# Kernel tuning notes

Measured on AMD Instinct MI355X. Metric: run time of the kernel, lower is better.

## Reference

```python
import jax, jax.numpy as jnp
import numpy as np

DIM = 512
HEADS = 8
DIM_HEAD = 64
INNER = HEADS * DIM_HEAD


def setup_inputs() -> dict:
    key = jax.random.key(0)
    k1, k2, k3, k4 = jax.random.split(key, 4)
    x = jax.random.normal(k1, (4, 8192, DIM), dtype=jnp.float32)
    # nn.Linear(dim, inner*3, bias=False): weight applied as x @ W^T; store transposed form [dim, 3*inner]
    w_qkv = jax.random.normal(k2, (DIM, 3 * INNER), dtype=jnp.float32) / np.sqrt(DIM)
    w_out = jax.random.normal(k3, (INNER, DIM), dtype=jnp.float32) / np.sqrt(INNER)
    b_out = jax.random.normal(k4, (DIM,), dtype=jnp.float32) * 0.01
    return {"x": x, "w_qkv": w_qkv, "w_out": w_out, "b_out": b_out}


def reference(x, w_qkv, w_out, b_out):
    b, n, d = x.shape
    qkv = x @ w_qkv  # [b, n, 3*inner]
    q, k, v = jnp.split(qkv, 3, axis=-1)

    def to_heads(t):
        return t.reshape(b, n, HEADS, DIM_HEAD).transpose(0, 2, 1, 3)  # [b,h,n,dh]

    q, k, v = map(to_heads, (q, k, v))
    q = jax.nn.elu(q) + 1.0
    k = jax.nn.elu(k) + 1.0
    # kv summary: [b,h,dh,dh]
    kv = jnp.einsum('bhnd,bhnm->bhdm', k, v)
    # normalizer z: [b,h,n]  (note: original does NOT apply self.scale)
    z = 1.0 / (jnp.einsum('bhnd,bhd->bhn', q, k.sum(axis=2)) + 1e-6)
    out = jnp.einsum('bhnd,bhdm->bhnm', q, kv) * z[..., None]  # [b,h,n,dh]
    out = out.transpose(0, 2, 1, 3).reshape(b, n, INNER)
    return out @ w_out + b_out
```

## Files before the change

### kernel.cpp

```cpp
#include <hip/hip_runtime.h>
#include <hip/hip_bf16.h>

#define B_SZ 4
#define SEQ 8192
#define DIM 512
#define HEADS 8
#define DH 64
#define INNER 512
#define QKV_COLS 1536
#define M_TOT (B_SZ * SEQ)
#define BHN (B_SZ * HEADS)

typedef __bf16 bf16x8 __attribute__((ext_vector_type(8)));
typedef __bf16 bf16x4 __attribute__((ext_vector_type(4)));
typedef float f32x4 __attribute__((ext_vector_type(4)));

__device__ __forceinline__ float elu1(float x) {
    return x > 0.f ? x + 1.f : __expf(x);
}

__device__ __forceinline__ void gl_lds16(const void* g, void* l) {
    __builtin_amdgcn_global_load_lds(
        (const __attribute__((address_space(1))) unsigned int*)g,
        (__attribute__((address_space(3))) unsigned int*)l, 16, 0, 0);
}

__global__ void convert_x(const float* __restrict__ x, __bf16* __restrict__ xb) {
    int id = blockIdx.x * 256 + threadIdx.x;
    float4 f = reinterpret_cast<const float4*>(x)[id];
    bf16x4 h = {(__bf16)f.x, (__bf16)f.y, (__bf16)f.z, (__bf16)f.w};
    reinterpret_cast<bf16x4*>(xb)[id] = h;
}

__global__ void convert_weights(const float* __restrict__ w_qkv,
                                const float* __restrict__ w_out,
                                __bf16* __restrict__ wqkv_t,
                                __bf16* __restrict__ wout_t) {
    int id = blockIdx.x * 256 + threadIdx.x;
    if (id < QKV_COLS * DIM) {
        int n = id / DIM, k = id % DIM;
        wqkv_t[id] = (__bf16)w_qkv[k * QKV_COLS + n];
    } else {
        int id2 = id - QKV_COLS * DIM;
        if (id2 < INNER * DIM) {
            int n = id2 / DIM, k = id2 % DIM;
            wout_t[id2] = (__bf16)w_out[k * DIM + n];
        }
    }
}

#define TSTR 136
__launch_bounds__(256, 2)
__global__ void gemm_qkv(const __bf16* __restrict__ xb,
                         const __bf16* __restrict__ wqkv_t,
                         __bf16* __restrict__ q_ws,
                         __bf16* __restrict__ kT_ws,
                         __bf16* __restrict__ vT_ws) {
    __shared__ __attribute__((aligned(16))) char smem[128 * TSTR * 2];
    __bf16* As = (__bf16*)smem;
    __bf16* Bs = (__bf16*)(smem + 16384);
    __bf16* T  = (__bf16*)smem;

    const int tid = threadIdx.x;
    const int wid = tid >> 6;
    const int lane = tid & 63;
    const int wm = wid >> 1, wn = wid & 1;
    const int lq = lane >> 4, lr = lane & 15;
    const int m0 = blockIdx.x * 128;
    const int n0 = blockIdx.y * 128;
    const int lrow = lane >> 3;
    const int lcol = (lane & 7) * 8;

    f32x4 acc[4][4] = {};

    for (int kb = 0; kb < DIM; kb += 64) {
#pragma unroll
        for (int t = 0; t < 4; ++t) {
            int qi = wid * 4 + t;
            int row = qi * 8 + lrow;
            gl_lds16(&xb[(size_t)(m0 + row) * DIM + kb + lcol], &As[qi * 512]);
            gl_lds16(&wqkv_t[(size_t)(n0 + row) * DIM + kb + lcol], &Bs[qi * 512]);
        }
        __syncthreads();
#pragma unroll
        for (int ks = 0; ks < 2; ++ks) {
            bf16x8 af[4], bfv[4];
#pragma unroll
            for (int i = 0; i < 4; ++i)
                af[i] = *reinterpret_cast<const bf16x8*>(
                    &As[(wm * 64 + i * 16 + lr) * 64 + ks * 32 + lq * 8]);
#pragma unroll
            for (int j = 0; j < 4; ++j)
                bfv[j] = *reinterpret_cast<const bf16x8*>(
                    &Bs[(wn * 64 + j * 16 + lr) * 64 + ks * 32 + lq * 8]);
#pragma unroll
            for (int i = 0; i < 4; ++i)
#pragma unroll
                for (int j = 0; j < 4; ++j)
                    acc[i][j] = __builtin_amdgcn_mfma_f32_16x16x32_bf16(
                        af[i], bfv[j], acc[i][j], 0, 0, 0);
        }
        __syncthreads();
    }

    const int which = n0 / INNER;
    const int n0w = n0 % INNER;
    const int b = m0 / SEQ;
    const int nbase = m0 % SEQ;

    if (which == 0) {
#pragma unroll
        for (int i = 0; i < 4; ++i)
#pragma unroll
            for (int j = 0; j < 4; ++j) {
                int col = wn * 64 + j * 16 + lr;
#pragma unroll
                for (int r = 0; r < 4; ++r)
                    T[(wm * 64 + i * 16 + lq * 4 + r) * TSTR + col] =
                        (__bf16)elu1(acc[i][j][r]);
            }
        __syncthreads();
#pragma unroll
        for (int it = 0; it < 8; ++it) {
            int c = tid + it * 256;
            int row = c >> 4, dc = (c & 15) * 8;
            bf16x8 v = *reinterpret_cast<const bf16x8*>(&T[row * TSTR + dc]);
            int col = n0w + dc;
            int h = col >> 6, d = col & 63;
            *reinterpret_cast<bf16x8*>(
                &q_ws[(((size_t)(b * HEADS + h)) * SEQ + nbase + row) * DH + d]) = v;
        }
    } else {
        __bf16* dst = (which == 1) ? kT_ws : vT_ws;
#pragma unroll
        for (int i = 0; i < 4; ++i)
#pragma unroll
            for (int j = 0; j < 4; ++j) {
                int col = wn * 64 + j * 16 + lr;
                int rowb = wm * 64 + i * 16 + lq * 4;
                bf16x4 h4;
#pragma unroll
                for (int r = 0; r < 4; ++r) {
                    float v = acc[i][j][r];
                    h4[r] = (__bf16)((which == 1) ? elu1(v) : v);
                }
                *reinterpret_cast<bf16x4*>(&T[col * TSTR + rowb]) = h4;
            }
        __syncthreads();
#pragma unroll
        for (int it = 0; it < 8; ++it) {
            int c = tid + it * 256;
            int colIdx = c >> 4, rc = (c & 15) * 8;
            bf16x8 v = *reinterpret_cast<const bf16x8*>(&T[colIdx * TSTR + rc]);
            int gcol = n0w + colIdx;
            int h = gcol >> 6, d = gcol & 63;
            *reinterpret_cast<bf16x8*>(
                &dst[(((size_t)(b * HEADS + h)) * DH + d) * SEQ + nbase + rc]) = v;
        }
    }
}

__launch_bounds__(256, 2)
__global__ void kv_reduce(const __bf16* __restrict__ kT,
                          const __bf16* __restrict__ vT,
                          float* __restrict__ kv_t) {
    __shared__ __attribute__((aligned(16))) __bf16 Ks[64][136];
    __shared__ __attribute__((aligned(16))) __bf16 Vs[64][136];
    const int tid = threadIdx.x;
    const int wid = tid >> 6;
    const int lane = tid & 63;
    const int lq = lane >> 4, lr = lane & 15;
    const int bh = blockIdx.y;
    const int n0 = blockIdx.x * 512;
    const size_t base = (size_t)bh * DH * SEQ;
    f32x4 acc[4] = {};

    for (int ch = 0; ch < 4; ++ch) {
        int nc = n0 + ch * 128;
#pragma unroll
        for (int t = 0; t < 4; ++t) {
            int c = tid + t * 256;
            int row = c >> 4, kc = (c & 15) * 8;
            *reinterpret_cast<bf16x8*>(&Ks[row][kc]) =
                *reinterpret_cast<const bf16x8*>(&kT[base + (size_t)row * SEQ + nc + kc]);
            *reinterpret_cast<bf16x8*>(&Vs[row][kc]) =
                *reinterpret_cast<const bf16x8*>(&vT[base + (size_t)row * SEQ + nc + kc]);
        }
        __syncthreads();
#pragma unroll
        for (int ks = 0; ks < 4; ++ks) {
            bf16x8 a = *reinterpret_cast<const bf16x8*>(&Ks[wid * 16 + lr][ks * 32 + lq * 8]);
#pragma unroll
            for (int j = 0; j < 4; ++j) {
                bf16x8 b = *reinterpret_cast<const bf16x8*>(&Vs[j * 16 + lr][ks * 32 + lq * 8]);
                acc[j] = __builtin_amdgcn_mfma_f32_16x16x32_bf16(a, b, acc[j], 0, 0, 0);
            }
        }
        __syncthreads();
    }
    float* dst = kv_t + (size_t)bh * DH * DH;
#pragma unroll
    for (int j = 0; j < 4; ++j) {
        int m = j * 16 + lr;
#pragma unroll
        for (int r = 0; r < 4; ++r) {
            int d = wid * 16 + lq * 4 + r;
            atomicAdd(&dst[m * DH + d], acc[j][r]);
        }
    }
}

__global__ void ksum_kernel(const __bf16* __restrict__ kT, float* __restrict__ ksum) {
    const int wid = threadIdx.x >> 6, lane = threadIdx.x & 63;
    const int row = blockIdx.x * 4 + wid;
    const __bf16* src = kT + (size_t)row * SEQ;
    float s = 0.f;
    for (int i = 0; i < 16; ++i) {
        bf16x8 v = *reinterpret_cast<const bf16x8*>(&src[(i * 64 + lane) * 8]);
#pragma unroll
        for (int j = 0; j < 8; ++j) s += (float)v[j];
    }
#pragma unroll
    for (int off = 32; off > 0; off >>= 1) s += __shfl_down(s, off, 64);
    if (lane == 0) ksum[row] = s;
}

__launch_bounds__(256, 2)
__global__ void attn_kernel(const __bf16* __restrict__ q_ws,
                            const float* __restrict__ kv_t,
                            const float* __restrict__ ksum,
                            __bf16* __restrict__ attn) {
    __shared__ __attribute__((aligned(16))) __bf16 Qs[128][72];
    __shared__ __attribute__((aligned(16))) __bf16 KVs[64][72];
    __shared__ float zs[128];
    __shared__ float ks_s[64];
    const int tid = threadIdx.x;
    const int wid = tid >> 6, lane = tid & 63;
    const int lq = lane >> 4, lr = lane & 15;
    const int bh = blockIdx.y;
    const int b = bh >> 3, h = bh & 7;
    const int n0 = blockIdx.x * 128;
    const size_t qbase = ((size_t)bh * SEQ + n0) * DH;

#pragma unroll
    for (int t = 0; t < 4; ++t) {
        int c = tid + t * 256;
        int row = c >> 3, kc = (c & 7) * 8;
        *reinterpret_cast<bf16x8*>(&Qs[row][kc]) =
            *reinterpret_cast<const bf16x8*>(&q_ws[qbase + (size_t)row * DH + kc]);
    }
    const float* kvsrc = kv_t + (size_t)bh * DH * DH;
#pragma unroll
    for (int t = 0; t < 4; ++t) {
        int c = tid + t * 256;
        int m = c >> 4, dc = (c & 15) * 4;
        float4 f = *reinterpret_cast<const float4*>(&kvsrc[m * DH + dc]);
        bf16x4 h4 = {(__bf16)f.x, (__bf16)f.y, (__bf16)f.z, (__bf16)f.w};
        *reinterpret_cast<bf16x4*>(&KVs[m][dc]) = h4;
    }
    if (tid < 64) ks_s[tid] = ksum[bh * DH + tid];
    __syncthreads();
    {
        int row = tid >> 1, part = tid & 1;
        float s = 0.f;
#pragma unroll
        for (int j = 0; j < 32; ++j)
            s += (float)Qs[row][part * 32 + j] * ks_s[part * 32 + j];
        s += __shfl_xor(s, 1, 64);
        if (part == 0) zs[row] = 1.f / (s + 1e-6f);
    }
    __syncthreads();

    f32x4 acc[2][4] = {};
#pragma unroll
    for (int ks = 0; ks < 2; ++ks) {
        bf16x8 a0 = *reinterpret_cast<const bf16x8*>(&Qs[wid * 32 + lr][ks * 32 + lq * 8]);
        bf16x8 a1 = *reinterpret_cast<const bf16x8*>(&Qs[wid * 32 + 16 + lr][ks * 32 + lq * 8]);
#pragma unroll
        for (int j = 0; j < 4; ++j) {
            bf16x8 bfr = *reinterpret_cast<const bf16x8*>(&KVs[j * 16 + lr][ks * 32 + lq * 8]);
            acc[0][j] = __builtin_amdgcn_mfma_f32_16x16x32_bf16(a0, bfr, acc[0][j], 0, 0, 0);
            acc[1][j] = __builtin_amdgcn_mfma_f32_16x16x32_bf16(a1, bfr, acc[1][j], 0, 0, 0);
        }
    }
#pragma unroll
    for (int mt = 0; mt < 2; ++mt)
#pragma unroll
        for (int j = 0; j < 4; ++j) {
            int m = j * 16 + lr;
#pragma unroll
            for (int r = 0; r < 4; ++r) {
                int row = wid * 32 + mt * 16 + lq * 4 + r;
                float v = acc[mt][j][r] * zs[row];
                attn[((size_t)(b * SEQ + n0 + row)) * INNER + h * DH + m] = (__bf16)v;
            }
        }
}

__launch_bounds__(256, 2)
__global__ void gemm_out(const __bf16* __restrict__ attn,
                         const __bf16* __restrict__ wout_t,
                         const float* __restrict__ b_out,
                         float* __restrict__ out) {
    __shared__ __attribute__((aligned(16))) char smem[32768];
    __bf16* As = (__bf16*)smem;
    __bf16* Bs = (__bf16*)(smem + 16384);

    const int tid = threadIdx.x;
    const int wid = tid >> 6;
    const int lane = tid & 63;
    const int wm = wid >> 1, wn = wid & 1;
    const int lq = lane >> 4, lr = lane & 15;
    const int m0 = blockIdx.x * 128;
    const int n0 = blockIdx.y * 128;
    const int lrow = lane >> 3;
    const int lcol = (lane & 7) * 8;

    f32x4 acc[4][4] = {};

    for (int kb = 0; kb < INNER; kb += 64) {
#pragma unroll
        for (int t = 0; t < 4; ++t) {
            int qi = wid * 4 + t;
            int row = qi * 8 + lrow;
            gl_lds16(&attn[(size_t)(m0 + row) * INNER + kb + lcol], &As[qi * 512]);
            gl_lds16(&wout_t[(size_t)(n0 + row) * INNER + kb + lcol], &Bs[qi * 512]);
        }
        __syncthreads();
#pragma unroll
        for (int ks = 0; ks < 2; ++ks) {
            bf16x8 af[4], bfv[4];
#pragma unroll
            for (int i = 0; i < 4; ++i)
                af[i] = *reinterpret_cast<const bf16x8*>(
                    &As[(wm * 64 + i * 16 + lr) * 64 + ks * 32 + lq * 8]);
#pragma unroll
            for (int j = 0; j < 4; ++j)
                bfv[j] = *reinterpret_cast<const bf16x8*>(
                    &Bs[(wn * 64 + j * 16 + lr) * 64 + ks * 32 + lq * 8]);
#pragma unroll
            for (int i = 0; i < 4; ++i)
#pragma unroll
                for (int j = 0; j < 4; ++j)
                    acc[i][j] = __builtin_amdgcn_mfma_f32_16x16x32_bf16(
                        af[i], bfv[j], acc[i][j], 0, 0, 0);
        }
        __syncthreads();
    }

#pragma unroll
    for (int j = 0; j < 4; ++j) {
        int col = n0 + wn * 64 + j * 16 + lr;
        float bias = b_out[col];
#pragma unroll
        for (int i = 0; i < 4; ++i) {
            int row = m0 + wm * 64 + i * 16 + lq * 4;
#pragma unroll
            for (int r = 0; r < 4; ++r)
                out[(size_t)(row + r) * DIM + col] = acc[i][j][r] + bias;
        }
    }
}

extern "C" void kernel_launch(void* const* d_in, const int* in_sizes, int n_in,
                              void* d_out, int out_size, void* d_ws, size_t ws_size,
                              hipStream_t stream) {
    (void)in_sizes; (void)n_in; (void)out_size; (void)ws_size;
    const float* x     = (const float*)d_in[0];
    const float* w_qkv = (const float*)d_in[1];
    const float* w_out = (const float*)d_in[2];
    const float* b_out = (const float*)d_in[3];
    float* out = (float*)d_out;

    char* ws = (char*)d_ws;
    size_t off = 0;
    auto alloc = [&](size_t bytes) {
        char* p = ws + off;
        off += (bytes + 255) & ~(size_t)255;
        return p;
    };
    __bf16* xb     = (__bf16*)alloc((size_t)M_TOT * DIM * 2);
    __bf16* attn   = xb;
    __bf16* q_ws   = (__bf16*)alloc((size_t)BHN * SEQ * DH * 2);
    __bf16* kT_ws  = (__bf16*)alloc((size_t)BHN * SEQ * DH * 2);
    __bf16* vT_ws  = (__bf16*)alloc((size_t)BHN * SEQ * DH * 2);
    float*  kv_t   = (float*)alloc((size_t)BHN * DH * DH * 4 + (size_t)BHN * DH * 4);
    float*  ksum   = kv_t + (size_t)BHN * DH * DH;
    __bf16* wqkv_t = (__bf16*)alloc((size_t)QKV_COLS * DIM * 2);
    __bf16* wout_t = (__bf16*)alloc((size_t)INNER * DIM * 2);

    hipMemsetAsync(kv_t, 0, (size_t)BHN * DH * DH * 4 + (size_t)BHN * DH * 4, stream);
    convert_x<<<dim3(M_TOT * DIM / 4 / 256), 256, 0, stream>>>(x, xb);
    convert_weights<<<dim3((QKV_COLS * DIM + INNER * DIM) / 256), 256, 0, stream>>>(
        w_qkv, w_out, wqkv_t, wout_t);
    gemm_qkv<<<dim3(M_TOT / 128, QKV_COLS / 128), 256, 0, stream>>>(
        xb, wqkv_t, q_ws, kT_ws, vT_ws);
    kv_reduce<<<dim3(16, BHN), 256, 0, stream>>>(kT_ws, vT_ws, kv_t);
    ksum_kernel<<<dim3(BHN * DH / 4), 256, 0, stream>>>(kT_ws, ksum);
    attn_kernel<<<dim3(SEQ / 128, BHN), 256, 0, stream>>>(q_ws, kv_t, ksum, attn);
    gemm_out<<<dim3(M_TOT / 128, DIM / 128), 256, 0, stream>>>(attn, wout_t, b_out, out);
}
```

Before: 302.7 us.

## Swizzle GEMM LDS tiles, fuse ksum into kv_reduce, merge conversion kernels, stage attn stores

Applies an XOR swizzle to the LDS tiles in both GEMMs so that MFMA fragment reads avoid bank conflicts. The k-sum is computed inside kv_reduce with an MFMA against a vector of ones, which removes the separate ksum kernel and its second pass over K. The x and weight conversion kernels are merged into a single launch. The attention output is staged through LDS so it is written to global memory as coalesced 16-byte stores, at the cost of two extra barriers and some extra atomics.

```diff
diff --git a/kernel.cpp b/kernel.cpp
--- a/kernel.cpp
+++ b/kernel.cpp
@@ -25,26 +25,29 @@
         (__attribute__((address_space(3))) unsigned int*)l, 16, 0, 0);
 }
 
-__global__ void convert_x(const float* __restrict__ x, __bf16* __restrict__ xb) {
+__global__ void convert_all(const float* __restrict__ x,
+                            const float* __restrict__ w_qkv,
+                            const float* __restrict__ w_out,
+                            __bf16* __restrict__ xb,
+                            __bf16* __restrict__ wqkv_t,
+                            __bf16* __restrict__ wout_t) {
+    const int NX = M_TOT * DIM / 4;
     int id = blockIdx.x * 256 + threadIdx.x;
-    float4 f = reinterpret_cast<const float4*>(x)[id];
-    bf16x4 h = {(__bf16)f.x, (__bf16)f.y, (__bf16)f.z, (__bf16)f.w};
-    reinterpret_cast<bf16x4*>(xb)[id] = h;
-}
-
-__global__ void convert_weights(const float* __restrict__ w_qkv,
-                                const float* __restrict__ w_out,
-                                __bf16* __restrict__ wqkv_t,
-                                __bf16* __restrict__ wout_t) {
-    int id = blockIdx.x * 256 + threadIdx.x;
-    if (id < QKV_COLS * DIM) {
-        int n = id / DIM, k = id % DIM;
-        wqkv_t[id] = (__bf16)w_qkv[k * QKV_COLS + n];
+    if (id < NX) {
+        float4 f = reinterpret_cast<const float4*>(x)[id];
+        bf16x4 h = {(__bf16)f.x, (__bf16)f.y, (__bf16)f.z, (__bf16)f.w};
+        reinterpret_cast<bf16x4*>(xb)[id] = h;
+        return;
+    }
+    int id2 = id - NX;
+    if (id2 < QKV_COLS * DIM) {
+        int n = id2 / DIM, k = id2 % DIM;
+        wqkv_t[id2] = (__bf16)w_qkv[k * QKV_COLS + n];
     } else {
-        int id2 = id - QKV_COLS * DIM;
-        if (id2 < INNER * DIM) {
-            int n = id2 / DIM, k = id2 % DIM;
-            wout_t[id2] = (__bf16)w_out[k * DIM + n];
+        int id3 = id2 - QKV_COLS * DIM;
+        if (id3 < INNER * DIM) {
+            int n = id3 / DIM, k = id3 % DIM;
+            wout_t[id3] = (__bf16)w_out[k * DIM + n];
         }
     }
 }
@@ -69,7 +72,7 @@
     const int m0 = blockIdx.x * 128;
     const int n0 = blockIdx.y * 128;
     const int lrow = lane >> 3;
-    const int lcol = (lane & 7) * 8;
+    const int lsw  = ((lane & 7) ^ lrow) * 8;
 
     f32x4 acc[4][4] = {};
 
@@ -78,21 +81,22 @@
         for (int t = 0; t < 4; ++t) {
             int qi = wid * 4 + t;
             int row = qi * 8 + lrow;
-            gl_lds16(&xb[(size_t)(m0 + row) * DIM + kb + lcol], &As[qi * 512]);
-            gl_lds16(&wqkv_t[(size_t)(n0 + row) * DIM + kb + lcol], &Bs[qi * 512]);
+            gl_lds16(&xb[(size_t)(m0 + row) * DIM + kb + lsw], &As[qi * 512]);
+            gl_lds16(&wqkv_t[(size_t)(n0 + row) * DIM + kb + lsw], &Bs[qi * 512]);
         }
         __syncthreads();
 #pragma unroll
         for (int ks = 0; ks < 2; ++ks) {
+            const int csw = ((ks * 4 + lq) ^ (lr & 7)) * 8;
             bf16x8 af[4], bfv[4];
 #pragma unroll
             for (int i = 0; i < 4; ++i)
                 af[i] = *reinterpret_cast<const bf16x8*>(
-                    &As[(wm * 64 + i * 16 + lr) * 64 + ks * 32 + lq * 8]);
+                    &As[(wm * 64 + i * 16 + lr) * 64 + csw]);
 #pragma unroll
             for (int j = 0; j < 4; ++j)
                 bfv[j] = *reinterpret_cast<const bf16x8*>(
-                    &Bs[(wn * 64 + j * 16 + lr) * 64 + ks * 32 + lq * 8]);
+                    &Bs[(wn * 64 + j * 16 + lr) * 64 + csw]);
 #pragma unroll
             for (int i = 0; i < 4; ++i)
 #pragma unroll
@@ -163,7 +167,8 @@
 __launch_bounds__(256, 2)
 __global__ void kv_reduce(const __bf16* __restrict__ kT,
                           const __bf16* __restrict__ vT,
-                          float* __restrict__ kv_t) {
+                          float* __restrict__ kv_t,
+                          float* __restrict__ ksum) {
     __shared__ __attribute__((aligned(16))) __bf16 Ks[64][136];
     __shared__ __attribute__((aligned(16))) __bf16 Vs[64][136];
     const int tid = threadIdx.x;
@@ -174,6 +179,10 @@
     const int n0 = blockIdx.x * 512;
     const size_t base = (size_t)bh * DH * SEQ;
     f32x4 acc[4] = {};
+    f32x4 acc1 = {};
+    bf16x8 ones8;
+#pragma unroll
+    for (int e = 0; e < 8; ++e) ones8[e] = (__bf16)1.f;
 
     for (int ch = 0; ch < 4; ++ch) {
         int nc = n0 + ch * 128;
@@ -190,6 +199,7 @@
 #pragma unroll
         for (int ks = 0; ks < 4; ++ks) {
             bf16x8 a = *reinterpret_cast<const bf16x8*>(&Ks[wid * 16 + lr][ks * 32 + lq * 8]);
+            acc1 = __builtin_amdgcn_mfma_f32_16x16x32_bf16(a, ones8, acc1, 0, 0, 0);
 #pragma unroll
             for (int j = 0; j < 4; ++j) {
                 bf16x8 b = *reinterpret_cast<const bf16x8*>(&Vs[j * 16 + lr][ks * 32 + lq * 8]);
@@ -208,21 +218,11 @@
             atomicAdd(&dst[m * DH + d], acc[j][r]);
         }
     }
-}
-
-__global__ void ksum_kernel(const __bf16* __restrict__ kT, float* __restrict__ ksum) {
-    const int wid = threadIdx.x >> 6, lane = threadIdx.x & 63;
-    const int row = blockIdx.x * 4 + wid;
-    const __bf16* src = kT + (size_t)row * SEQ;
-    float s = 0.f;
-    for (int i = 0; i < 16; ++i) {
-        bf16x8 v = *reinterpret_cast<const bf16x8*>(&src[(i * 64 + lane) * 8]);
-#pragma unroll
-        for (int j = 0; j < 8; ++j) s += (float)v[j];
-    }
-#pragma unroll
-    for (int off = 32; off > 0; off >>= 1) s += __shfl_down(s, off, 64);
-    if (lane == 0) ksum[row] = s;
+    if (lr == 0) {
+#pragma unroll
+        for (int r = 0; r < 4; ++r)
+            atomicAdd(&ksum[bh * DH + wid * 16 + lq * 4 + r], acc1[r]);
+    }
 }
 
 __launch_bounds__(256, 2)
@@ -283,6 +283,7 @@
             acc[1][j] = __builtin_amdgcn_mfma_f32_16x16x32_bf16(a1, bfr, acc[1][j], 0, 0, 0);
         }
     }
+    __syncthreads();
 #pragma unroll
     for (int mt = 0; mt < 2; ++mt)
 #pragma unroll
@@ -291,10 +292,18 @@
 #pragma unroll
             for (int r = 0; r < 4; ++r) {
                 int row = wid * 32 + mt * 16 + lq * 4 + r;
-                float v = acc[mt][j][r] * zs[row];
-                attn[((size_t)(b * SEQ + n0 + row)) * INNER + h * DH + m] = (__bf16)v;
+                Qs[row][m] = (__bf16)(acc[mt][j][r] * zs[row]);
             }
         }
+    __syncthreads();
+#pragma unroll
+    for (int it = 0; it < 4; ++it) {
+        int c = tid + it * 256;
+        int row = c >> 3, mc = (c & 7) * 8;
+        bf16x8 v = *reinterpret_cast<const bf16x8*>(&Qs[row][mc]);
+        *reinterpret_cast<bf16x8*>(
+            &attn[((size_t)(b * SEQ + n0 + row)) * INNER + h * DH + mc]) = v;
+    }
 }
 
 __launch_bounds__(256, 2)
@@ -314,7 +323,7 @@
     const int m0 = blockIdx.x * 128;
     const int n0 = blockIdx.y * 128;
     const int lrow = lane >> 3;
-    const int lcol = (lane & 7) * 8;
+    const int lsw  = ((lane & 7) ^ lrow) * 8;
 
     f32x4 acc[4][4] = {};
 
@@ -323,21 +332,22 @@
         for (int t = 0; t < 4; ++t) {
             int qi = wid * 4 + t;
             int row = qi * 8 + lrow;
-            gl_lds16(&attn[(size_t)(m0 + row) * INNER + kb + lcol], &As[qi * 512]);
-            gl_lds16(&wout_t[(size_t)(n0 + row) * INNER + kb + lcol], &Bs[qi * 512]);
+            gl_lds16(&attn[(size_t)(m0 + row) * INNER + kb + lsw], &As[qi * 512]);
+            gl_lds16(&wout_t[(size_t)(n0 + row) * INNER + kb + lsw], &Bs[qi * 512]);
         }
         __syncthreads();
 #pragma unroll
         for (int ks = 0; ks < 2; ++ks) {
+            const int csw = ((ks * 4 + lq) ^ (lr & 7)) * 8;
             bf16x8 af[4], bfv[4];
 #pragma unroll
             for (int i = 0; i < 4; ++i)
                 af[i] = *reinterpret_cast<const bf16x8*>(
-                    &As[(wm * 64 + i * 16 + lr) * 64 + ks * 32 + lq * 8]);
+                    &As[(wm * 64 + i * 16 + lr) * 64 + csw]);
 #pragma unroll
             for (int j = 0; j < 4; ++j)
                 bfv[j] = *reinterpret_cast<const bf16x8*>(
-                    &Bs[(wn * 64 + j * 16 + lr) * 64 + ks * 32 + lq * 8]);
+                    &Bs[(wn * 64 + j * 16 + lr) * 64 + csw]);
 #pragma unroll
             for (int i = 0; i < 4; ++i)
 #pragma unroll
@@ -390,13 +400,11 @@
     __bf16* wout_t = (__bf16*)alloc((size_t)INNER * DIM * 2);
 
     hipMemsetAsync(kv_t, 0, (size_t)BHN * DH * DH * 4 + (size_t)BHN * DH * 4, stream);
-    convert_x<<<dim3(M_TOT * DIM / 4 / 256), 256, 0, stream>>>(x, xb);
-    convert_weights<<<dim3((QKV_COLS * DIM + INNER * DIM) / 256), 256, 0, stream>>>(
-        w_qkv, w_out, wqkv_t, wout_t);
+    convert_all<<<dim3(M_TOT * DIM / 4 / 256 + (QKV_COLS * DIM + INNER * DIM) / 256),
+                  256, 0, stream>>>(x, w_qkv, w_out, xb, wqkv_t, wout_t);
     gemm_qkv<<<dim3(M_TOT / 128, QKV_COLS / 128), 256, 0, stream>>>(
         xb, wqkv_t, q_ws, kT_ws, vT_ws);
-    kv_reduce<<<dim3(16, BHN), 256, 0, stream>>>(kT_ws, vT_ws, kv_t);
-    ksum_kernel<<<dim3(BHN * DH / 4), 256, 0, stream>>>(kT_ws, ksum);
+    kv_reduce<<<dim3(16, BHN), 256, 0, stream>>>(kT_ws, vT_ws, kv_t, ksum);
     attn_kernel<<<dim3(SEQ / 128, BHN), 256, 0, stream>>>(q_ws, kv_t, ksum, attn);
     gemm_out<<<dim3(M_TOT / 128, DIM / 128), 256, 0, stream>>>(attn, wout_t, b_out, out);
 }
```

New measurement: 267.0 us. 11.8% less time.
